# Kernel optimization log

Hardware: AMD Instinct MI355X
Metric: run time of the kernel (lower is better)

Reference implementation:

```python
import jax, jax.numpy as jnp
import numpy as np

N_NODES = 100000
DIM = 256
N_SAMPLES = 64
N_CLASSES = 10


def setup_inputs() -> dict:
    key = jax.random.key(0)
    k1, k2, k3 = jax.random.split(key, 3)
    data = jax.random.normal(k1, (N_SAMPLES, DIM), dtype=jnp.float32)
    V = jax.random.uniform(k2, (N_NODES, DIM), dtype=jnp.float32)  # node matrix (torch.rand init)
    labels = jax.random.randint(k3, (N_SAMPLES,), 0, N_CLASSES)
    return {"data": data, "V": V, "labels": labels, "it": 0}


def reference(data, V, labels, it):
    # SOINN+ per-sample BMU search + BMU/sBMU weight pull, fixed node capacity.
    # eps schedules exactly as in ASOINN.forward.
    eps_b = 1.0 / (it + 2)
    eps_n = 1.0 / ((it + 1) * 100)

    def step(Vc, sample):
        # pairwise L2 distance of sample vs all nodes: [N]
        diff = sample[None, :] - Vc
        dists = jnp.sqrt(jnp.sum(diff * diff, axis=-1) + 1e-12)
        neg_vals, idx = jax.lax.top_k(-dists, 2)  # two smallest
        b, s = idx[0], idx[1]
        # update_bmu: V[b] += eps_b * (sample - V[b]); neighbor pull on sBMU
        Vc = Vc.at[b].add(eps_b * (sample - Vc[b]))
        Vc = Vc.at[s].add(eps_n * (sample - Vc[s]))
        return Vc, -neg_vals  # (b_dist, s_dist)

    V_final, bmu_dists = jax.lax.scan(step, V, data)
    return bmu_dists  # [N_SAMPLES, 2]
```

## Files before the change

### kernel.cpp

```cpp
#include <hip/hip_runtime.h>
#include <math.h>


#define N_NODES 100000
#define DIM     256
#define NS      64
#define NCH     1563
#define KC      32
#define NBMW    3125
#define CAP     4096
#define KL      192
#define KLS     136

typedef unsigned long long u64;

__device__ __forceinline__ u64 pk(float d, int i) {
  return ((u64)__float_as_uint(d) << 32) | (unsigned)i;
}
__device__ __forceinline__ u64 umin64(u64 a, u64 b) { return a < b ? a : b; }
__device__ __forceinline__ u64 umax64(u64 a, u64 b) { return a > b ? a : b; }
__device__ __forceinline__ void mrg2(u64& A0, u64& A1, u64 B0, u64 B1) {
  u64 m = umax64(A0, B0);
  A0 = umin64(A0, B0);
  A1 = umin64(umin64(A1, B1), m);
}

template <int C>
__device__ __forceinline__ u64 dpp64(u64 x) {
  unsigned lo = (unsigned)__builtin_amdgcn_update_dpp(
      (int)0xFFFFFFFF, (int)(unsigned)(x & 0xFFFFFFFFull), C, 0xF, 0xF, false);
  unsigned hi = (unsigned)__builtin_amdgcn_update_dpp(
      (int)0xFFFFFFFF, (int)(unsigned)(x >> 32), C, 0xF, 0xF, false);
  return ((u64)hi << 32) | lo;
}
template <int C>
__device__ __forceinline__ void dpp_round(u64& A0, u64& A1) {
  u64 B0 = dpp64<C>(A0);
  u64 B1 = dpp64<C>(A1);
  mrg2(A0, A1, B0, B1);
}

__global__ void k_xx(const float* __restrict__ X, float* __restrict__ XX) {
  int i = blockIdx.x, j = threadIdx.x;
  const float* xi = X + i * DIM;
  const float* xj = X + j * DIM;
  float acc = 0.f;
  for (int k = 0; k < DIM; k += 4) {
    float4 a = *(const float4*)(xi + k);
    float4 b = *(const float4*)(xj + k);
    acc += a.x * b.x + a.y * b.y + a.z * b.z + a.w * b.w;
  }
  XX[i * NS + j] = acc;
}

__global__ __launch_bounds__(256) void k_dist(const float* __restrict__ X,
                                              const float* __restrict__ V,
                                              const float* __restrict__ XX,
                                              float* __restrict__ P,
                                              float* __restrict__ PT,
                                              float* __restrict__ Q,
                                              u64* __restrict__ SUMC) {
  __shared__ float Xl[KC][68];
  __shared__ float Vl[KC][136];
  __shared__ float sq[128];
  const int tid = threadIdx.x;
  const int n0  = blockIdx.x * 128;
  const int ty  = tid >> 5;
  const int tx  = tid & 31;
  float acc[8][4];
#pragma unroll
  for (int i = 0; i < 8; i++)
#pragma unroll
    for (int u = 0; u < 4; u++) acc[i][u] = 0.f;
  float qa = 0.f;
  const int xsl = tid & 63;
  const int xkk = (tid >> 6) * 8;
  const int vn  = tid & 127;
  const int vkk = (tid >> 7) * 16;

  for (int kc = 0; kc < DIM; kc += KC) {
    __syncthreads();
#pragma unroll
    for (int m = 0; m < 2; m++) {
      float4 x = *(const float4*)(X + xsl * DIM + kc + xkk + 4 * m);
      Xl[xkk + 4 * m + 0][xsl] = x.x; Xl[xkk + 4 * m + 1][xsl] = x.y;
      Xl[xkk + 4 * m + 2][xsl] = x.z; Xl[xkk + 4 * m + 3][xsl] = x.w;
    }
    {
      int n = n0 + vn;
      bool ok = (n < N_NODES);
      const float* vp = V + (size_t)n * DIM + kc + vkk;
#pragma unroll
      for (int m = 0; m < 4; m++) {
        float4 v = ok ? *(const float4*)(vp + 4 * m) : make_float4(0.f, 0.f, 0.f, 0.f);
        Vl[vkk + 4 * m + 0][vn] = v.x; Vl[vkk + 4 * m + 1][vn] = v.y;
        Vl[vkk + 4 * m + 2][vn] = v.z; Vl[vkk + 4 * m + 3][vn] = v.w;
      }
    }
    __syncthreads();
    if (tid < 128) {
      float qq = 0.f;
#pragma unroll 8
      for (int k = 0; k < KC; k++) { float t = Vl[k][tid]; qq += t * t; }
      qa += qq;
    }
#pragma unroll 4
    for (int k = 0; k < KC; k++) {
      float xs[8], vs[4];
      *(float4*)&xs[0] = *(const float4*)&Xl[k][ty * 8];
      *(float4*)&xs[4] = *(const float4*)&Xl[k][ty * 8 + 4];
      *(float4*)&vs[0] = *(const float4*)&Vl[k][tx * 4];
#pragma unroll
      for (int i = 0; i < 8; i++)
#pragma unroll
        for (int u = 0; u < 4; u++) acc[i][u] += xs[i] * vs[u];
    }
  }
  if (tid < 128) sq[tid] = qa;
  __syncthreads();
  if (tid < 128 && n0 + tid < N_NODES) Q[n0 + tid] = qa;
  float qs[4];
  *(float4*)&qs[0] = *(const float4*)&sq[tx * 4];
  const bool full = (n0 + 128) <= N_NODES;
#pragma unroll
  for (int i = 0; i < 8; i++) {
    int s = ty * 8 + i;
    float xn = XX[s * NS + s];
#pragma unroll
    for (int u = 0; u < 4; u++) acc[i][u] = xn - 2.f * acc[i][u] + qs[u];
    float* prow = P + (size_t)s * N_NODES + n0 + tx * 4;
    if (full) {
      *(float4*)(prow) = make_float4(acc[i][0], acc[i][1], acc[i][2], acc[i][3]);
    } else {
#pragma unroll
      for (int u = 0; u < 4; u++) {
        int n = n0 + tx * 4 + u;
        if (n < N_NODES) prow[u] = acc[i][u];
      }
    }
  }
#pragma unroll
  for (int u = 0; u < 4; u++) {
    int n = n0 + tx * 4 + u;
    if (n < N_NODES) {
      float* pt = PT + (size_t)n * NS + ty * 8;
      *(float4*)(pt)     = make_float4(acc[0][u], acc[1][u], acc[2][u], acc[3][u]);
      *(float4*)(pt + 4) = make_float4(acc[4][u], acc[5][u], acc[6][u], acc[7][u]);
    }
  }
#pragma unroll
  for (int i = 0; i < 8; i++) {
    int s = ty * 8 + i;
    u64 key = ~0ull;
#pragma unroll
    for (int u = 0; u < 4; u++) {
      int n = n0 + tx * 4 + u;
      if (n < N_NODES) key = umin64(key, pk(acc[i][u], n));
    }
#pragma unroll
    for (int off = 1; off <= 8; off <<= 1)
      key = umin64(key, (u64)__shfl_xor((unsigned long long)key, off, 64));
    if ((tx & 15) == 0) {
      int chunk = (n0 >> 6) + (tx >> 4);
      if (chunk < NCH) SUMC[(size_t)s * NCH + chunk] = key;
    }
  }
}

__global__ __launch_bounds__(1024) void k_build(const u64* __restrict__ SUMC,
                                                const float* __restrict__ P,
                                                u64* __restrict__ L) {
  __shared__ u64 A[CAP];
  __shared__ float Tsh;
  __shared__ int cnt;
  const int j = blockIdx.x, tid = threadIdx.x;
  for (int i = tid; i < 2048; i += 1024)
    A[i] = (i < NCH) ? SUMC[(size_t)j * NCH + i] : ~0ull;
  __syncthreads();
  for (int k = 2; k <= 2048; k <<= 1)
    for (int s2 = k >> 1; s2 > 0; s2 >>= 1) {
      for (int i = tid; i < 2048; i += 1024) {
        int p = i ^ s2;
        if (p > i) {
          u64 a = A[i], b = A[p];
          bool up = ((i & k) == 0);
          if ((a > b) == up) { A[i] = b; A[p] = a; }
        }
      }
      __syncthreads();
    }
  if (tid == 0) {
    Tsh = __uint_as_float((unsigned)(A[159] >> 32));
    cnt = 0;
  }
  __syncthreads();
  const float T = Tsh;
  __syncthreads();
  const float* prow = P + (size_t)j * N_NODES;
  for (int n0 = tid * 4; n0 < N_NODES + 3; n0 += 4096) {
    float d[4];
    if (n0 + 3 < N_NODES) {
      float4 p = *(const float4*)(prow + n0);
      d[0] = p.x; d[1] = p.y; d[2] = p.z; d[3] = p.w;
    } else {
#pragma unroll
      for (int e = 0; e < 4; e++)
        d[e] = (n0 + e < N_NODES) ? prow[n0 + e] : INFINITY;
    }
#pragma unroll
    for (int e = 0; e < 4; e++) {
      if (d[e] <= T) {
        int pos = atomicAdd(&cnt, 1);
        if (pos < CAP) A[pos] = pk(d[e], n0 + e);
      }
    }
  }
  __syncthreads();
  int n = cnt; if (n > CAP) n = CAP;
  int M = 256; while (M < n) M <<= 1;
  for (int i = tid; i < M; i += 1024)
    if (i >= n) A[i] = ~0ull;
  __syncthreads();
  for (int k = 2; k <= M; k <<= 1)
    for (int s2 = k >> 1; s2 > 0; s2 >>= 1) {
      for (int i = tid; i < M; i += 1024) {
        int p = i ^ s2;
        if (p > i) {
          u64 a = A[i], b = A[p];
          bool up = ((i & k) == 0);
          if ((a > b) == up) { A[i] = b; A[p] = a; }
        }
      }
      __syncthreads();
    }
  for (int i = tid; i < KL; i += 1024) L[(size_t)j * KL + i] = A[i];
}

__global__ __launch_bounds__(192) void k_seq(
    const float* __restrict__ PT, const float* __restrict__ Q,
    const float* __restrict__ XXg, const u64* __restrict__ L,
    const int* __restrict__ itp, float* __restrict__ out) {
  __shared__ u64 Lsh[NS][KLS];
  __shared__ float XXl[NS * 65];
  __shared__ float g[128][65];
  __shared__ float qv[128];
  __shared__ unsigned int bitmap[NBMW];
  __shared__ int tracked[128];
  __shared__ u64 verd[NS][3];
  __shared__ float specg[4][4][NS];
  __shared__ float specq[4][4];
  __shared__ int   specid[4][4];
  __shared__ int ready[NS];
  __shared__ int done[NS];

  const int tid = threadIdx.x;
  const int wv = tid >> 6;
  const int lane = tid & 63;

  for (int i = tid; i < NS * KLS; i += 192) {
    int r = i / KLS, c = i - r * KLS;
    Lsh[r][c] = L[(size_t)r * KL + c];
  }
  for (int i = tid; i < NS * NS; i += 192) {
    int r = i >> 6, c = i & 63;
    XXl[r * 65 + c] = XXg[i];
  }
  for (int i = tid; i < NBMW; i += 192) bitmap[i] = 0u;
  for (int i = tid; i < NS; i += 192) { ready[i] = 0; done[i] = 0; }
  __syncthreads();

  const int it = itp[0];
  const float eps_b = 1.0f / (float)(it + 2);
  const float eps_n = 1.0f / (float)((it + 1) * 100);
  const float xdl = XXl[lane * 65 + lane];

  if (wv == 0) {
    int ns = 0, pr0 = -1, pr1 = -1;
    for (int j = 0; j < NS; j++) {
      while (__hip_atomic_load(&ready[j], __ATOMIC_ACQUIRE,
                               __HIP_MEMORY_SCOPE_WORKGROUP) == 0)
        __builtin_amdgcn_s_sleep(1);
      const int sb = j & 3;
      u64 k0 = Lsh[j][lane], k1 = Lsh[j][lane + 64];
      u64 k2 = (lane < 8) ? Lsh[j][128 + lane] : ~0ull;
      u64 vm0 = verd[j][0], vm1 = verd[j][1], vm2 = verd[j][2];
      float gA = g[lane][j], gB = g[lane + 64][j];
      float qvA = qv[lane],  qvB = qv[lane + 64];
      int   tA = tracked[lane], tB = tracked[lane + 64];
      float sg0 = specg[sb][0][lane], sg1 = specg[sb][1][lane];
      float sg2 = specg[sb][2][lane], sg3 = specg[sb][3][lane];
      int sid0 = specid[sb][0], sid1 = specid[sb][1];
      int sid2 = specid[sb][2], sid3 = specid[sb][3];
      float sq0 = specq[sb][0], sq1 = specq[sb][1];
      float sq2 = specq[sb][2], sq3 = specq[sb][3];
      float xrow = XXl[j * 65 + lane];
      float xnj = __uint_as_float(
          (unsigned)__builtin_amdgcn_readlane((int)__float_as_uint(xrow), j));
      u64 A0 = ~0ull, A1 = ~0ull;
      {
        int i0 = (int)(unsigned)(k0 & 0xFFFFFFFFull);
        int i1 = (int)(unsigned)(k1 & 0xFFFFFFFFull);
        int i2 = (int)(unsigned)(k2 & 0xFFFFFFFFull);
        if (!((vm0 >> lane) & 1ull) && i0 != pr0 && i0 != pr1) mrg2(A0, A1, k0, ~0ull);
        if (!((vm1 >> lane) & 1ull) && i1 != pr0 && i1 != pr1) mrg2(A0, A1, k1, ~0ull);
        if (!((vm2 >> lane) & 1ull) && i2 != pr0 && i2 != pr1) mrg2(A0, A1, k2, ~0ull);
      }
      if (lane < ns)      { float d = xnj - 2.f * gA + qvA; mrg2(A0, A1, pk(d, tA), ~0ull); }
      if (lane + 64 < ns) { float d = xnj - 2.f * gB + qvB; mrg2(A0, A1, pk(d, tB), ~0ull); }
      dpp_round<0x111>(A0, A1);
      dpp_round<0x112>(A0, A1);
      dpp_round<0x114>(A0, A1);
      dpp_round<0x118>(A0, A1);
      dpp_round<0x142>(A0, A1);
      dpp_round<0x143>(A0, A1);
      const int r0 = (int)(unsigned)__builtin_amdgcn_readlane(
          (int)(unsigned)(A0 & 0xFFFFFFFFull), 63);
      const int r1 = (int)(unsigned)__builtin_amdgcn_readlane(
          (int)(unsigned)(A1 & 0xFFFFFFFFull), 63);
      if (lane == 63) {
        float2 o;
        o.x = sqrtf(fmaxf(__uint_as_float((unsigned)(A0 >> 32)), 0.f) + 1e-12f);
        o.y = sqrtf(fmaxf(__uint_as_float((unsigned)(A1 >> 32)), 0.f) + 1e-12f);
        *(float2*)(out + j * 2) = o;
      }
      bool h0a = (lane < ns) && (tA == r0);
      bool h0b = (lane + 64 < ns) && (tB == r0);
      u64 mk0a = __ballot(h0a), mk0b = __ballot(h0b);
      bool new0 = (mk0a | mk0b) == 0ull;
      int sl0 = new0 ? ns
                     : (mk0a ? (__ffsll((unsigned long long)mk0a) - 1)
                             : (64 + __ffsll((unsigned long long)mk0b) - 1));
      bool h1a = (lane < ns) && (tA == r1);
      bool h1b = (lane + 64 < ns) && (tB == r1);
      u64 mk1a = __ballot(h1a), mk1b = __ballot(h1b);
      bool new1 = (mk1a | mk1b) == 0ull;
      int sl1 = new1 ? (ns + (new0 ? 1 : 0))
                     : (mk1a ? (__ffsll((unsigned long long)mk1a) - 1)
                             : (64 + __ffsll((unsigned long long)mk1b) - 1));
      bool m00 = (sid0 == r0), m01 = (sid1 == r0), m02 = (sid2 == r0), m03 = (sid3 == r0);
      bool hit0 = m00 | m01 | m02 | m03;
      float pv0 = m00 ? sg0 : m01 ? sg1 : m02 ? sg2 : sg3;
      float qq0 = m00 ? sq0 : m01 ? sq1 : m02 ? sq2 : sq3;
      bool m10 = (sid0 == r1), m11 = (sid1 == r1), m12 = (sid2 == r1), m13 = (sid3 == r1);
      bool hit1 = m10 | m11 | m12 | m13;
      float pv1 = m10 ? sg0 : m11 ? sg1 : m12 ? sg2 : sg3;
      float qq1 = m10 ? sq0 : m11 ? sq1 : m12 ? sq2 : sq3;
      if (new0 && !hit0) { pv0 = PT[(size_t)r0 * NS + lane]; qq0 = Q[r0]; }
      if (new1 && !hit1) { pv1 = PT[(size_t)r1 * NS + lane]; qq1 = Q[r1]; }
      float gt0 = g[sl0][lane];
      float gt1 = g[sl1][lane];
      float gold0 = new0 ? (0.5f * (xdl + qq0 - pv0)) : gt0;
      float qold0 = new0 ? qq0
                         : __uint_as_float((unsigned)__builtin_amdgcn_readlane(
                               (int)__float_as_uint(sl0 < 64 ? qvA : qvB), sl0 & 63));
      float gj0 = __uint_as_float(
          (unsigned)__builtin_amdgcn_readlane((int)__float_as_uint(gold0), j));
      g[sl0][lane] = (1.f - eps_b) * gold0 + eps_b * xrow;
      if (lane == 0) {
        float om = 1.f - eps_b;
        qv[sl0] = om * om * qold0 + 2.f * eps_b * om * gj0 + eps_b * eps_b * xnj;
        tracked[sl0] = r0;
        if (new0) bitmap[r0 >> 5] |= 1u << (r0 & 31);
      }
      float gold1 = new1 ? (0.5f * (xdl + qq1 - pv1)) : gt1;
      float qold1 = new1 ? qq1
                         : __uint_as_float((unsigned)__builtin_amdgcn_readlane(
                               (int)__float_as_uint(sl1 < 64 ? qvA : qvB), sl1 & 63));
      float gj1 = __uint_as_float(
          (unsigned)__builtin_amdgcn_readlane((int)__float_as_uint(gold1), j));
      g[sl1][lane] = (1.f - eps_n) * gold1 + eps_n * xrow;
      if (lane == 0) {
        float on = 1.f - eps_n;
        qv[sl1] = on * on * qold1 + 2.f * eps_n * on * gj1 + eps_n * eps_n * xnj;
        tracked[sl1] = r1;
        if (new1) bitmap[r1 >> 5] |= 1u << (r1 & 31);
      }
      ns += (new0 ? 1 : 0) + (new1 ? 1 : 0);
      pr0 = r0; pr1 = r1;
      __hip_atomic_store(&done[j], 1, __ATOMIC_RELEASE,
                         __HIP_MEMORY_SCOPE_WORKGROUP);
    }
  } else {
    for (int t = (wv == 1 ? 0 : 1); t < NS; t += 2) {
      if (t >= 2) {
        while (__hip_atomic_load(&done[t - 2], __ATOMIC_ACQUIRE,
                                 __HIP_MEMORY_SCOPE_WORKGROUP) == 0)
          __builtin_amdgcn_s_sleep(1);
      }
      u64 e0 = Lsh[t][lane], e1 = Lsh[t][lane + 64];
      u64 e2 = (lane < 8) ? Lsh[t][128 + lane] : ~0ull;
      int i0 = (int)(unsigned)(e0 & 0xFFFFFFFFull);
      int i1 = (int)(unsigned)(e1 & 0xFFFFFFFFull);
      int i2 = (int)(unsigned)(e2 & 0xFFFFFFFFull);
      bool t0 = (e0 == ~0ull) || ((bitmap[i0 >> 5] >> (i0 & 31)) & 1u);
      bool t1 = (e1 == ~0ull) || ((bitmap[i1 >> 5] >> (i1 & 31)) & 1u);
      bool t2 = (e2 == ~0ull) || ((bitmap[i2 >> 5] >> (i2 & 31)) & 1u);
      u64 m0 = __ballot(t0), m1 = __ballot(t1), m2 = __ballot(t2);
      if (lane == 0) { verd[t][0] = m0; verd[t][1] = m1; verd[t][2] = m2; }
      u64 um[3] = {~m0, ~m1, ~m2};
      int posk[4] = {0, 0, 0, 0};
      int pcnt = 0;
#pragma unroll
      for (int gi = 0; gi < 3; gi++) {
        u64 mm = um[gi];
        while (mm && pcnt < 4) {
          int b2 = __ffsll((unsigned long long)mm) - 1;
          posk[pcnt++] = gi * 64 + b2;
          mm &= mm - 1;
        }
      }
      int id0 = (int)(unsigned)(Lsh[t][posk[0]] & 0xFFFFFFFFull);
      int id1 = (int)(unsigned)(Lsh[t][posk[1]] & 0xFFFFFFFFull);
      int id2 = (int)(unsigned)(Lsh[t][posk[2]] & 0xFFFFFFFFull);
      int id3 = (int)(unsigned)(Lsh[t][posk[3]] & 0xFFFFFFFFull);
      float p0 = PT[(size_t)id0 * NS + lane], p1 = PT[(size_t)id1 * NS + lane];
      float p2 = PT[(size_t)id2 * NS + lane], p3 = PT[(size_t)id3 * NS + lane];
      const int sb = t & 3;
      specg[sb][0][lane] = p0; specg[sb][1][lane] = p1;
      specg[sb][2][lane] = p2; specg[sb][3][lane] = p3;
      if (lane == 0) {
        specid[sb][0] = id0; specid[sb][1] = id1;
        specid[sb][2] = id2; specid[sb][3] = id3;
        specq[sb][0] = Q[id0]; specq[sb][1] = Q[id1];
        specq[sb][2] = Q[id2]; specq[sb][3] = Q[id3];
      }
      __hip_atomic_store(&ready[t], 1, __ATOMIC_RELEASE,
                         __HIP_MEMORY_SCOPE_WORKGROUP);
    }
  }
}

extern "C" void kernel_launch(void* const* d_in, const int* in_sizes, int n_in,
                              void* d_out, int out_size, void* d_ws, size_t ws_size,
                              hipStream_t stream) {
  const float* X  = (const float*)d_in[0];
  const float* V  = (const float*)d_in[1];
  const int*  itp = (const int*)d_in[3];
  float* out = (float*)d_out;

  char* ws = (char*)d_ws;
  size_t off = 0;
  auto alloc = [&](size_t bytes) -> void* {
    size_t o = (off + 255) & ~(size_t)255;
    off = o + bytes;
    return (void*)(ws + o);
  };
  float* P    = (float*)alloc((size_t)NS * N_NODES * sizeof(float));
  float* PT   = (float*)alloc((size_t)NS * N_NODES * sizeof(float));
  float* Q    = (float*)alloc((size_t)N_NODES * sizeof(float));
  float* XXp  = (float*)alloc((size_t)NS * NS * sizeof(float));
  u64*   SUMC = (u64*)alloc((size_t)NS * NCH * sizeof(u64));
  u64*   Lst  = (u64*)alloc((size_t)NS * KL * sizeof(u64));

  k_xx   <<<NS, NS, 0, stream>>>(X, XXp);
  k_dist <<<(N_NODES + 127) / 128, 256, 0, stream>>>(X, V, XXp, P, PT, Q, SUMC);
  k_build<<<NS, 1024, 0, stream>>>(SUMC, P, Lst);
  k_seq  <<<1, 192, 0, stream>>>(PT, Q, XXp, Lst, itp, out);
}
```

Baseline: 340.6 us.

## Enlarge distance tile, prefetch registers, replace bitonic threshold, streamline sequential candidate handoff

k_dist now covers 256 nodes per block with an 8x8 register tile per thread. Each thread loads a whole V row slice into registers and prefetches the next K chunk while computing the current one, and it accumulates norms from registers. k_build replaces the 2048-element bitonic sort used to find the threshold with per-wave iterative min extraction. k_seq drops the Lsh staging: helper waves read L directly, compact up to 16 untracked candidates via popcount ranks, and speculate 6 PT rows with a deeper lookahead. The changes raise register pressure and change the candidate-exclusion logic, which could affect occupancy or correctness.

```diff
diff --git a/kernel.cpp b/kernel.cpp
--- a/kernel.cpp
+++ b/kernel.cpp
@@ -61,87 +61,103 @@
                                               float* __restrict__ Q,
                                               u64* __restrict__ SUMC) {
   __shared__ float Xl[KC][68];
-  __shared__ float Vl[KC][136];
-  __shared__ float sq[128];
+  __shared__ float Vl[KC][264];
+  __shared__ float sq[256];
   const int tid = threadIdx.x;
-  const int n0  = blockIdx.x * 128;
+  const int n0  = blockIdx.x * 256;
   const int ty  = tid >> 5;
   const int tx  = tid & 31;
-  float acc[8][4];
+  float acc[8][8];
 #pragma unroll
   for (int i = 0; i < 8; i++)
 #pragma unroll
-    for (int u = 0; u < 4; u++) acc[i][u] = 0.f;
+    for (int u = 0; u < 8; u++) acc[i][u] = 0.f;
   float qa = 0.f;
   const int xsl = tid & 63;
   const int xkk = (tid >> 6) * 8;
-  const int vn  = tid & 127;
-  const int vkk = (tid >> 7) * 16;
-
-  for (int kc = 0; kc < DIM; kc += KC) {
+  const int vn  = n0 + tid;
+  const bool vok = (vn < N_NODES);
+  const float* vrow = V + (size_t)vn * DIM;
+  const float* xrow = X + xsl * DIM + xkk;
+
+  float4 xr0, xr1, vr[8];
+  xr0 = *(const float4*)(xrow + 0);
+  xr1 = *(const float4*)(xrow + 4);
+#pragma unroll
+  for (int m = 0; m < 8; m++)
+    vr[m] = vok ? *(const float4*)(vrow + 4 * m) : make_float4(0.f, 0.f, 0.f, 0.f);
+
+  for (int c = 0; c < 8; c++) {
     __syncthreads();
-#pragma unroll
-    for (int m = 0; m < 2; m++) {
-      float4 x = *(const float4*)(X + xsl * DIM + kc + xkk + 4 * m);
-      Xl[xkk + 4 * m + 0][xsl] = x.x; Xl[xkk + 4 * m + 1][xsl] = x.y;
-      Xl[xkk + 4 * m + 2][xsl] = x.z; Xl[xkk + 4 * m + 3][xsl] = x.w;
+    Xl[xkk + 0][xsl] = xr0.x; Xl[xkk + 1][xsl] = xr0.y;
+    Xl[xkk + 2][xsl] = xr0.z; Xl[xkk + 3][xsl] = xr0.w;
+    Xl[xkk + 4][xsl] = xr1.x; Xl[xkk + 5][xsl] = xr1.y;
+    Xl[xkk + 6][xsl] = xr1.z; Xl[xkk + 7][xsl] = xr1.w;
+#pragma unroll
+    for (int m = 0; m < 8; m++) {
+      Vl[4 * m + 0][tid] = vr[m].x; Vl[4 * m + 1][tid] = vr[m].y;
+      Vl[4 * m + 2][tid] = vr[m].z; Vl[4 * m + 3][tid] = vr[m].w;
     }
     {
-      int n = n0 + vn;
-      bool ok = (n < N_NODES);
-      const float* vp = V + (size_t)n * DIM + kc + vkk;
-#pragma unroll
-      for (int m = 0; m < 4; m++) {
-        float4 v = ok ? *(const float4*)(vp + 4 * m) : make_float4(0.f, 0.f, 0.f, 0.f);
-        Vl[vkk + 4 * m + 0][vn] = v.x; Vl[vkk + 4 * m + 1][vn] = v.y;
-        Vl[vkk + 4 * m + 2][vn] = v.z; Vl[vkk + 4 * m + 3][vn] = v.w;
-      }
+      float qq = 0.f;
+#pragma unroll
+      for (int m = 0; m < 8; m++) {
+        qq += vr[m].x * vr[m].x; qq += vr[m].y * vr[m].y;
+        qq += vr[m].z * vr[m].z; qq += vr[m].w * vr[m].w;
+      }
+      qa += qq;
     }
     __syncthreads();
-    if (tid < 128) {
-      float qq = 0.f;
-#pragma unroll 8
-      for (int k = 0; k < KC; k++) { float t = Vl[k][tid]; qq += t * t; }
-      qa += qq;
+    if (c + 1 < 8) {
+      int kc = (c + 1) * KC;
+      xr0 = *(const float4*)(xrow + kc);
+      xr1 = *(const float4*)(xrow + kc + 4);
+#pragma unroll
+      for (int m = 0; m < 8; m++)
+        vr[m] = vok ? *(const float4*)(vrow + kc + 4 * m)
+                    : make_float4(0.f, 0.f, 0.f, 0.f);
     }
 #pragma unroll 4
     for (int k = 0; k < KC; k++) {
-      float xs[8], vs[4];
+      float xs[8], vs[8];
       *(float4*)&xs[0] = *(const float4*)&Xl[k][ty * 8];
       *(float4*)&xs[4] = *(const float4*)&Xl[k][ty * 8 + 4];
-      *(float4*)&vs[0] = *(const float4*)&Vl[k][tx * 4];
+      *(float4*)&vs[0] = *(const float4*)&Vl[k][tx * 8];
+      *(float4*)&vs[4] = *(const float4*)&Vl[k][tx * 8 + 4];
 #pragma unroll
       for (int i = 0; i < 8; i++)
 #pragma unroll
-        for (int u = 0; u < 4; u++) acc[i][u] += xs[i] * vs[u];
-    }
-  }
-  if (tid < 128) sq[tid] = qa;
-  __syncthreads();
-  if (tid < 128 && n0 + tid < N_NODES) Q[n0 + tid] = qa;
-  float qs[4];
-  *(float4*)&qs[0] = *(const float4*)&sq[tx * 4];
-  const bool full = (n0 + 128) <= N_NODES;
+        for (int u = 0; u < 8; u++) acc[i][u] += xs[i] * vs[u];
+    }
+  }
+  sq[tid] = qa;
+  __syncthreads();
+  if (vok) Q[vn] = qa;
+  float qs[8];
+  *(float4*)&qs[0] = *(const float4*)&sq[tx * 8];
+  *(float4*)&qs[4] = *(const float4*)&sq[tx * 8 + 4];
+  const bool full = (n0 + 256) <= N_NODES;
 #pragma unroll
   for (int i = 0; i < 8; i++) {
     int s = ty * 8 + i;
     float xn = XX[s * NS + s];
 #pragma unroll
-    for (int u = 0; u < 4; u++) acc[i][u] = xn - 2.f * acc[i][u] + qs[u];
-    float* prow = P + (size_t)s * N_NODES + n0 + tx * 4;
+    for (int u = 0; u < 8; u++) acc[i][u] = xn - 2.f * acc[i][u] + qs[u];
+    float* prow = P + (size_t)s * N_NODES + n0 + tx * 8;
     if (full) {
-      *(float4*)(prow) = make_float4(acc[i][0], acc[i][1], acc[i][2], acc[i][3]);
+      *(float4*)(prow)     = make_float4(acc[i][0], acc[i][1], acc[i][2], acc[i][3]);
+      *(float4*)(prow + 4) = make_float4(acc[i][4], acc[i][5], acc[i][6], acc[i][7]);
     } else {
 #pragma unroll
-      for (int u = 0; u < 4; u++) {
-        int n = n0 + tx * 4 + u;
+      for (int u = 0; u < 8; u++) {
+        int n = n0 + tx * 8 + u;
         if (n < N_NODES) prow[u] = acc[i][u];
       }
     }
   }
 #pragma unroll
-  for (int u = 0; u < 4; u++) {
-    int n = n0 + tx * 4 + u;
+  for (int u = 0; u < 8; u++) {
+    int n = n0 + tx * 8 + u;
     if (n < N_NODES) {
       float* pt = PT + (size_t)n * NS + ty * 8;
       *(float4*)(pt)     = make_float4(acc[0][u], acc[1][u], acc[2][u], acc[3][u]);
@@ -153,15 +169,15 @@
     int s = ty * 8 + i;
     u64 key = ~0ull;
 #pragma unroll
-    for (int u = 0; u < 4; u++) {
-      int n = n0 + tx * 4 + u;
+    for (int u = 0; u < 8; u++) {
+      int n = n0 + tx * 8 + u;
       if (n < N_NODES) key = umin64(key, pk(acc[i][u], n));
     }
 #pragma unroll
-    for (int off = 1; off <= 8; off <<= 1)
+    for (int off = 1; off <= 4; off <<= 1)
       key = umin64(key, (u64)__shfl_xor((unsigned long long)key, off, 64));
-    if ((tx & 15) == 0) {
-      int chunk = (n0 >> 6) + (tx >> 4);
+    if ((tx & 7) == 0) {
+      int chunk = (n0 >> 6) + (tx >> 3);
       if (chunk < NCH) SUMC[(size_t)s * NCH + chunk] = key;
     }
   }
@@ -171,31 +187,39 @@
                                                 const float* __restrict__ P,
                                                 u64* __restrict__ L) {
   __shared__ u64 A[CAP];
+  __shared__ u64 Twave[16];
   __shared__ float Tsh;
   __shared__ int cnt;
   const int j = blockIdx.x, tid = threadIdx.x;
-  for (int i = tid; i < 2048; i += 1024)
-    A[i] = (i < NCH) ? SUMC[(size_t)j * NCH + i] : ~0ull;
-  __syncthreads();
-  for (int k = 2; k <= 2048; k <<= 1)
-    for (int s2 = k >> 1; s2 > 0; s2 >>= 1) {
-      for (int i = tid; i < 2048; i += 1024) {
-        int p = i ^ s2;
-        if (p > i) {
-          u64 a = A[i], b = A[p];
-          bool up = ((i & k) == 0);
-          if ((a > b) == up) { A[i] = b; A[p] = a; }
-        }
-      }
-      __syncthreads();
-    }
+  const int w = tid >> 6, l = tid & 63;
+  {
+    int base = w * 98;
+    u64 v0 = (base + l < NCH) ? SUMC[(size_t)j * NCH + base + l] : ~0ull;
+    u64 v1 = (l < 34 && base + 64 + l < NCH)
+                 ? SUMC[(size_t)j * NCH + base + 64 + l] : ~0ull;
+    u64 s9 = ~0ull;
+#pragma unroll
+    for (int r = 0; r < 9; r++) {
+      u64 m = umin64(v0, v1);
+#pragma unroll
+      for (int off = 1; off <= 32; off <<= 1)
+        m = umin64(m, (u64)__shfl_xor((unsigned long long)m, off, 64));
+      if (r == 8) { s9 = m; } else {
+        if (v0 == m) v0 = ~0ull;
+        if (v1 == m) v1 = ~0ull;
+      }
+    }
+    if (l == 0) Twave[w] = s9;
+  }
+  __syncthreads();
   if (tid == 0) {
-    Tsh = __uint_as_float((unsigned)(A[159] >> 32));
+    u64 t = 0;
+    for (int i = 0; i < 16; i++) t = umax64(t, Twave[i]);
+    Tsh = __uint_as_float((unsigned)(t >> 32));
     cnt = 0;
   }
   __syncthreads();
   const float T = Tsh;
-  __syncthreads();
   const float* prow = P + (size_t)j * N_NODES;
   for (int n0 = tid * 4; n0 < N_NODES + 3; n0 += 4096) {
     float d[4];
@@ -233,23 +257,22 @@
       }
       __syncthreads();
     }
-  for (int i = tid; i < KL; i += 1024) L[(size_t)j * KL + i] = A[i];
+  for (int i = tid; i < KLS; i += 1024) L[(size_t)j * KL + i] = A[i];
 }
 
 __global__ __launch_bounds__(192) void k_seq(
     const float* __restrict__ PT, const float* __restrict__ Q,
     const float* __restrict__ XXg, const u64* __restrict__ L,
     const int* __restrict__ itp, float* __restrict__ out) {
-  __shared__ u64 Lsh[NS][KLS];
   __shared__ float XXl[NS * 65];
   __shared__ float g[128][65];
   __shared__ float qv[128];
   __shared__ unsigned int bitmap[NBMW];
   __shared__ int tracked[128];
-  __shared__ u64 verd[NS][3];
-  __shared__ float specg[4][4][NS];
-  __shared__ float specq[4][4];
-  __shared__ int   specid[4][4];
+  __shared__ u64 cand16[NS][16];
+  __shared__ float specg[4][6][NS];
+  __shared__ float specq[4][6];
+  __shared__ int   specid[4][6];
   __shared__ int ready[NS];
   __shared__ int done[NS];
 
@@ -257,10 +280,6 @@
   const int wv = tid >> 6;
   const int lane = tid & 63;
 
-  for (int i = tid; i < NS * KLS; i += 192) {
-    int r = i / KLS, c = i - r * KLS;
-    Lsh[r][c] = L[(size_t)r * KL + c];
-  }
   for (int i = tid; i < NS * NS; i += 192) {
     int r = i >> 6, c = i & 63;
     XXl[r * 65 + c] = XXg[i];
@@ -275,35 +294,31 @@
   const float xdl = XXl[lane * 65 + lane];
 
   if (wv == 0) {
-    int ns = 0, pr0 = -1, pr1 = -1;
+    int ns = 0;
+    int pw0 = -1, pw1 = -1, pw2 = -1, pw3 = -1;
     for (int j = 0; j < NS; j++) {
       while (__hip_atomic_load(&ready[j], __ATOMIC_ACQUIRE,
                                __HIP_MEMORY_SCOPE_WORKGROUP) == 0)
         __builtin_amdgcn_s_sleep(1);
       const int sb = j & 3;
-      u64 k0 = Lsh[j][lane], k1 = Lsh[j][lane + 64];
-      u64 k2 = (lane < 8) ? Lsh[j][128 + lane] : ~0ull;
-      u64 vm0 = verd[j][0], vm1 = verd[j][1], vm2 = verd[j][2];
+      u64 ck = (lane < 16) ? cand16[j][lane] : ~0ull;
+      float sgv[6], sqv[6]; int sid[6];
+#pragma unroll
+      for (int s = 0; s < 6; s++) {
+        sgv[s] = specg[sb][s][lane];
+        sid[s] = specid[sb][s];
+        sqv[s] = specq[sb][s];
+      }
       float gA = g[lane][j], gB = g[lane + 64][j];
       float qvA = qv[lane],  qvB = qv[lane + 64];
       int   tA = tracked[lane], tB = tracked[lane + 64];
-      float sg0 = specg[sb][0][lane], sg1 = specg[sb][1][lane];
-      float sg2 = specg[sb][2][lane], sg3 = specg[sb][3][lane];
-      int sid0 = specid[sb][0], sid1 = specid[sb][1];
-      int sid2 = specid[sb][2], sid3 = specid[sb][3];
-      float sq0 = specq[sb][0], sq1 = specq[sb][1];
-      float sq2 = specq[sb][2], sq3 = specq[sb][3];
       float xrow = XXl[j * 65 + lane];
-      float xnj = __uint_as_float(
-          (unsigned)__builtin_amdgcn_readlane((int)__float_as_uint(xrow), j));
+      float xnj  = XXl[j * 65 + j];
       u64 A0 = ~0ull, A1 = ~0ull;
       {
-        int i0 = (int)(unsigned)(k0 & 0xFFFFFFFFull);
-        int i1 = (int)(unsigned)(k1 & 0xFFFFFFFFull);
-        int i2 = (int)(unsigned)(k2 & 0xFFFFFFFFull);
-        if (!((vm0 >> lane) & 1ull) && i0 != pr0 && i0 != pr1) mrg2(A0, A1, k0, ~0ull);
-        if (!((vm1 >> lane) & 1ull) && i1 != pr0 && i1 != pr1) mrg2(A0, A1, k1, ~0ull);
-        if (!((vm2 >> lane) & 1ull) && i2 != pr0 && i2 != pr1) mrg2(A0, A1, k2, ~0ull);
+        int id = (int)(unsigned)(ck & 0xFFFFFFFFull);
+        bool ok = (ck != ~0ull) && id != pw0 && id != pw1 && id != pw2 && id != pw3;
+        if (ok) { A0 = ck; }
       }
       if (lane < ns)      { float d = xnj - 2.f * gA + qvA; mrg2(A0, A1, pk(d, tA), ~0ull); }
       if (lane + 64 < ns) { float d = xnj - 2.f * gB + qvB; mrg2(A0, A1, pk(d, tB), ~0ull); }
@@ -337,14 +352,14 @@
       int sl1 = new1 ? (ns + (new0 ? 1 : 0))
                      : (mk1a ? (__ffsll((unsigned long long)mk1a) - 1)
                              : (64 + __ffsll((unsigned long long)mk1b) - 1));
-      bool m00 = (sid0 == r0), m01 = (sid1 == r0), m02 = (sid2 == r0), m03 = (sid3 == r0);
-      bool hit0 = m00 | m01 | m02 | m03;
-      float pv0 = m00 ? sg0 : m01 ? sg1 : m02 ? sg2 : sg3;
-      float qq0 = m00 ? sq0 : m01 ? sq1 : m02 ? sq2 : sq3;
-      bool m10 = (sid0 == r1), m11 = (sid1 == r1), m12 = (sid2 == r1), m13 = (sid3 == r1);
-      bool hit1 = m10 | m11 | m12 | m13;
-      float pv1 = m10 ? sg0 : m11 ? sg1 : m12 ? sg2 : sg3;
-      float qq1 = m10 ? sq0 : m11 ? sq1 : m12 ? sq2 : sq3;
+      bool hit0 = false, hit1 = false;
+      float pv0 = 0.f, qq0 = 0.f, pv1 = 0.f, qq1 = 0.f;
+#pragma unroll
+      for (int s = 0; s < 6; s++) {
+        bool h0 = (sid[s] == r0), h1 = (sid[s] == r1);
+        pv0 = h0 ? sgv[s] : pv0;  qq0 = h0 ? sqv[s] : qq0;  hit0 |= h0;
+        pv1 = h1 ? sgv[s] : pv1;  qq1 = h1 ? sqv[s] : qq1;  hit1 |= h1;
+      }
       if (new0 && !hit0) { pv0 = PT[(size_t)r0 * NS + lane]; qq0 = Q[r0]; }
       if (new1 && !hit1) { pv1 = PT[(size_t)r1 * NS + lane]; qq1 = Q[r1]; }
       float gt0 = g[sl0][lane];
@@ -376,53 +391,49 @@
         if (new1) bitmap[r1 >> 5] |= 1u << (r1 & 31);
       }
       ns += (new0 ? 1 : 0) + (new1 ? 1 : 0);
-      pr0 = r0; pr1 = r1;
+      pw2 = pw0; pw3 = pw1; pw0 = r0; pw1 = r1;
       __hip_atomic_store(&done[j], 1, __ATOMIC_RELEASE,
                          __HIP_MEMORY_SCOPE_WORKGROUP);
     }
   } else {
     for (int t = (wv == 1 ? 0 : 1); t < NS; t += 2) {
-      if (t >= 2) {
-        while (__hip_atomic_load(&done[t - 2], __ATOMIC_ACQUIRE,
+      if (t >= 3) {
+        while (__hip_atomic_load(&done[t - 3], __ATOMIC_ACQUIRE,
                                  __HIP_MEMORY_SCOPE_WORKGROUP) == 0)
           __builtin_amdgcn_s_sleep(1);
       }
-      u64 e0 = Lsh[t][lane], e1 = Lsh[t][lane + 64];
-      u64 e2 = (lane < 8) ? Lsh[t][128 + lane] : ~0ull;
+      const u64* Lr = L + (size_t)t * KL;
+      u64 e0 = Lr[lane], e1 = Lr[lane + 64];
+      u64 e2 = (lane < 8) ? Lr[128 + lane] : ~0ull;
       int i0 = (int)(unsigned)(e0 & 0xFFFFFFFFull);
       int i1 = (int)(unsigned)(e1 & 0xFFFFFFFFull);
       int i2 = (int)(unsigned)(e2 & 0xFFFFFFFFull);
       bool t0 = (e0 == ~0ull) || ((bitmap[i0 >> 5] >> (i0 & 31)) & 1u);
       bool t1 = (e1 == ~0ull) || ((bitmap[i1 >> 5] >> (i1 & 31)) & 1u);
       bool t2 = (e2 == ~0ull) || ((bitmap[i2 >> 5] >> (i2 & 31)) & 1u);
-      u64 m0 = __ballot(t0), m1 = __ballot(t1), m2 = __ballot(t2);
-      if (lane == 0) { verd[t][0] = m0; verd[t][1] = m1; verd[t][2] = m2; }
-      u64 um[3] = {~m0, ~m1, ~m2};
-      int posk[4] = {0, 0, 0, 0};
-      int pcnt = 0;
-#pragma unroll
-      for (int gi = 0; gi < 3; gi++) {
-        u64 mm = um[gi];
-        while (mm && pcnt < 4) {
-          int b2 = __ffsll((unsigned long long)mm) - 1;
-          posk[pcnt++] = gi * 64 + b2;
-          mm &= mm - 1;
-        }
-      }
-      int id0 = (int)(unsigned)(Lsh[t][posk[0]] & 0xFFFFFFFFull);
-      int id1 = (int)(unsigned)(Lsh[t][posk[1]] & 0xFFFFFFFFull);
-      int id2 = (int)(unsigned)(Lsh[t][posk[2]] & 0xFFFFFFFFull);
-      int id3 = (int)(unsigned)(Lsh[t][posk[3]] & 0xFFFFFFFFull);
-      float p0 = PT[(size_t)id0 * NS + lane], p1 = PT[(size_t)id1 * NS + lane];
-      float p2 = PT[(size_t)id2 * NS + lane], p3 = PT[(size_t)id3 * NS + lane];
+      u64 um0 = ~__ballot(t0), um1 = ~__ballot(t1), um2 = ~__ballot(t2);
+      u64 below = (1ull << lane) - 1;
+      int c0n = __popcll((unsigned long long)um0);
+      int c1n = __popcll((unsigned long long)um1);
+      int rank0 = __popcll((unsigned long long)(um0 & below));
+      int rank1 = c0n + __popcll((unsigned long long)(um1 & below));
+      int rank2 = c0n + c1n + __popcll((unsigned long long)(um2 & below));
+      if (!t0 && rank0 < 16) cand16[t][rank0] = e0;
+      if (!t1 && rank1 < 16) cand16[t][rank1] = e1;
+      if (!t2 && rank2 < 16) cand16[t][rank2] = e2;
+      int U = c0n + c1n + __popcll((unsigned long long)um2);
+      if (lane < 16 && lane >= U) cand16[t][lane] = ~0ull;
       const int sb = t & 3;
-      specg[sb][0][lane] = p0; specg[sb][1][lane] = p1;
-      specg[sb][2][lane] = p2; specg[sb][3][lane] = p3;
-      if (lane == 0) {
-        specid[sb][0] = id0; specid[sb][1] = id1;
-        specid[sb][2] = id2; specid[sb][3] = id3;
-        specq[sb][0] = Q[id0]; specq[sb][1] = Q[id1];
-        specq[sb][2] = Q[id2]; specq[sb][3] = Q[id3];
+      int ids[6];
+#pragma unroll
+      for (int s = 0; s < 6; s++)
+        ids[s] = (int)(unsigned)(cand16[t][s] & 0xFFFFFFFFull);
+#pragma unroll
+      for (int s = 0; s < 6; s++)
+        specg[sb][s][lane] = PT[(size_t)ids[s] * NS + lane];
+      if (lane < 6) {
+        specid[sb][lane] = ids[lane];
+        specq[sb][lane] = Q[ids[lane]];
       }
       __hip_atomic_store(&ready[t], 1, __ATOMIC_RELEASE,
                          __HIP_MEMORY_SCOPE_WORKGROUP);
@@ -453,7 +464,7 @@
   u64*   Lst  = (u64*)alloc((size_t)NS * KL * sizeof(u64));
 
   k_xx   <<<NS, NS, 0, stream>>>(X, XXp);
-  k_dist <<<(N_NODES + 127) / 128, 256, 0, stream>>>(X, V, XXp, P, PT, Q, SUMC);
+  k_dist <<<(N_NODES + 255) / 256, 256, 0, stream>>>(X, V, XXp, P, PT, Q, SUMC);
   k_build<<<NS, 1024, 0, stream>>>(SUMC, P, Lst);
   k_seq  <<<1, 192, 0, stream>>>(PT, Q, XXp, Lst, itp, out);
 }
```

After: 316.2 us. -7.2%, faster.
